# Kernel tuning notes

Hardware: AMD Instinct MI355X
Metric: run time of the kernel (lower is better)

## Reference

```python
import jax, jax.numpy as jnp
import numpy as np


def _conv(x, w, b=None, stride=1, pad=0):
    y = jax.lax.conv_general_dilated(x, w, (stride, stride), [(pad, pad), (pad, pad)],
                                     dimension_numbers=('NCHW', 'OIHW', 'NCHW'))
    if b is not None:
        y = y + b[None, :, None, None]
    return y


def _slice3d(grid, guide):
    # Trilinear grid_sample, align_corners=False, zero padding.
    # grid: (N, C=12, D=8, GH, GW); guide: (N,1,H,W) in [-1,1]
    N, C, D, GH, GW = grid.shape
    H, W = guide.shape[2], guide.shape[3]
    xs = 2.0 * jnp.arange(W, dtype=grid.dtype) / max(W - 1, 1) - 1.0
    ys = 2.0 * jnp.arange(H, dtype=grid.dtype) / max(H - 1, 1) - 1.0
    gx = ((xs + 1.0) * GW - 1.0) * 0.5               # (W,)
    gy = ((ys + 1.0) * GH - 1.0) * 0.5               # (H,)
    gz = ((guide[:, 0] + 1.0) * D - 1.0) * 0.5       # (N,H,W)
    x0f = jnp.floor(gx); y0f = jnp.floor(gy); z0f = jnp.floor(gz)
    fx = gx - x0f; fy = gy - y0f; fz = gz - z0f
    x0 = x0f.astype(jnp.int32); y0 = y0f.astype(jnp.int32); z0 = z0f.astype(jnp.int32)
    gf = grid.reshape(N, C, D * GH * GW)

    def corner(zi, yi, xi, wz, wy, wx):
        mask = ((zi >= 0) & (zi < D)) & ((yi >= 0) & (yi < GH))[None, :, None] & ((xi >= 0) & (xi < GW))[None, None, :]
        zc = jnp.clip(zi, 0, D - 1); yc = jnp.clip(yi, 0, GH - 1); xc = jnp.clip(xi, 0, GW - 1)
        flat = zc * (GH * GW) + yc[None, :, None] * GW + xc[None, None, :]   # (N,H,W)
        v = jnp.take_along_axis(gf, flat.reshape(N, 1, H * W), axis=2).reshape(N, C, H, W)
        w = (wz * wy[None, :, None] * wx[None, None, :]) * mask.astype(grid.dtype)  # (N,H,W)
        return v * w[:, None]

    out = jnp.zeros((N, C, H, W), grid.dtype)
    for dz in (0, 1):
        for dy in (0, 1):
            for dx in (0, 1):
                out = out + corner(z0 + dz, y0 + dy, x0 + dx,
                                   fz if dz else 1.0 - fz,
                                   fy if dy else 1.0 - fy,
                                   fx if dx else 1.0 - fx)
    return out


def setup_inputs() -> dict:
    key = jax.random.key(0)
    ks = jax.random.split(key, 40)
    def w(i, shape):
        return jax.random.normal(ks[i], shape, jnp.float32) * 0.05
    return {
        'low_res': jax.random.uniform(ks[0], (4, 3, 256, 256), jnp.float32),
        'full_res': jax.random.uniform(ks[1], (4, 1, 1024, 1024), jnp.float32),
        'w0': w(2, (8, 3, 3, 3)), 'b0': w(3, (8,)),
        'w1': w(4, (16, 8, 3, 3)), 'b1': w(5, (16,)),
        'w2': w(6, (32, 16, 3, 3)), 'b2': w(7, (32,)),
        'w3': w(8, (64, 32, 3, 3)), 'b3': w(9, (64,)),
        'wl0': w(10, (64, 64, 3, 3)), 'bl0': w(11, (64,)),
        'wl1': w(12, (64, 64, 3, 3)),
        'wg1': w(13, (128, 64, 3, 3)), 'bg1': w(14, (128,)),
        'wg2': w(15, (256, 128, 3, 3)), 'bg2': w(16, (256,)),
        'wf1': w(17, (256, 448, 1, 1)), 'bf1': w(18, (256,)),
        'wf2': w(19, (128, 256, 1, 1)), 'bf2': w(20, (128,)),
        'wf3': w(21, (64, 128, 1, 1)), 'bf3': w(22, (64,)),
        'wlin': w(23, (96, 64, 1, 1)), 'blin': w(24, (96,)),
        'wgd1': w(25, (16, 1, 3, 3)), 'bgd1': w(26, (16,)),
        'wgd2': w(27, (1, 16, 1, 1)), 'bgd2': w(28, (1,)),
        'wau1': w(29, (16, 1, 1, 1)), 'bau1': w(30, (16,)),
        'wau2': w(31, (1, 16, 1, 1)), 'bau2': w(32, (1,)),
        'wav1': w(33, (16, 1, 1, 1)), 'bav1': w(34, (16,)),
        'wav2': w(35, (1, 16, 1, 1)), 'bav2': w(36, (1,)),
    }


def reference(low_res, full_res, w0, b0, w1, b1, w2, b2, w3, b3, wl0, bl0, wl1,
              wg1, bg1, wg2, bg2, wf1, bf1, wf2, bf2, wf3, bf3, wlin, blin,
              wgd1, bgd1, wgd2, bgd2, wau1, bau1, wau2, bau2, wav1, bav1, wav2, bav2):
    relu = jax.nn.relu
    N = low_res.shape[0]
    H, W = full_res.shape[2], full_res.shape[3]
    fake = jax.image.resize(low_res, (N, 3, H, W), 'bilinear')
    # splat stack: 4 stride-2 convs
    x = relu(_conv(low_res, w0, b0, 2, 1))
    x = relu(_conv(x, w1, b1, 2, 1))
    x = relu(_conv(x, w2, b2, 2, 1))
    splat = relu(_conv(x, w3, b3, 2, 1))                 # (N,64,16,16)
    local = _conv(relu(_conv(splat, wl0, bl0, 1, 1)), wl1, None, 1, 1)
    # global branch
    a0 = splat.mean(axis=(2, 3), keepdims=True)
    x1 = relu(_conv(splat, wg1, bg1, 2, 1))
    a1 = x1.mean(axis=(2, 3), keepdims=True)
    x2 = relu(_conv(x1, wg2, bg2, 2, 1))
    a2 = x2.mean(axis=(2, 3), keepdims=True)
    a = jnp.concatenate([a0, a1, a2], axis=1)            # (N,448,1,1)
    a = relu(_conv(a, wf1, bf1))
    a = relu(_conv(a, wf2, bf2))
    glob = relu(_conv(a, wf3, bf3))                      # (N,64,1,1)
    fused = relu(glob + local)
    fused = _conv(fused, wlin, blin)                     # (N,96,16,16)
    grid = fused.reshape(N, 12, 8, fused.shape[2], fused.shape[3])
    guidemap = jnp.tanh(_conv(relu(_conv(full_res, wgd1, bgd1, 1, 1)), wgd2, bgd2))
    coeff = _slice3d(grid, guidemap)                     # (N,12,H,W)
    Y = full_res * coeff[:, 3:4] + coeff[:, 0:3].sum(axis=1, keepdims=True)
    U0 = full_res * coeff[:, 7:8] + coeff[:, 4:7].sum(axis=1, keepdims=True)
    V0 = full_res * coeff[:, 11:12] + coeff[:, 8:11].sum(axis=1, keepdims=True)
    U = jnp.tanh(_conv(relu(_conv(U0, wau1, bau1)), wau2, bau2)) + fake[:, 1:2]
    V = jnp.tanh(_conv(relu(_conv(V0, wav1, bav1)), wav2, bav2)) + fake[:, 2:3]
    return jnp.concatenate([Y, U, V], axis=1)
```

## Files before the change

### kernel.cpp

```cpp
#include <hip/hip_runtime.h>
#include <math.h>


__device__ __forceinline__ float tanh_fast(float x) {
    float e = __expf(2.0f * x);
    return 1.0f - 2.0f / (e + 1.0f);
}

template<int CIN, int COUT, int HIN, int WIN, int HOUT, int WOUT>
__global__ __launch_bounds__(256) void conv_s2_small(
    const float* __restrict__ in, const float* __restrict__ w,
    const float* __restrict__ b, float* __restrict__ out)
{
    int idx = blockIdx.x * 256 + threadIdx.x;
    int wo = idx % WOUT; int t = idx / WOUT;
    int ho = t % HOUT; t /= HOUT;
    int co = t % COUT; int n = t / COUT;
    float acc = b[co];
    int hi0 = ho * 2 - 1, wi0 = wo * 2 - 1;
    const float* wp = w + (size_t)co * CIN * 9;
    #pragma unroll
    for (int ci = 0; ci < CIN; ++ci) {
        const float* ip = in + ((size_t)(n * CIN + ci)) * HIN * WIN;
        const float* wc = wp + ci * 9;
        #pragma unroll
        for (int kh = 0; kh < 3; ++kh) {
            int hi = hi0 + kh;
            if ((unsigned)hi >= (unsigned)HIN) continue;
            const float* row = ip + hi * WIN;
            #pragma unroll
            for (int kw = 0; kw < 3; ++kw) {
                int wi = wi0 + kw;
                if ((unsigned)wi >= (unsigned)WIN) continue;
                acc = fmaf(wc[kh * 3 + kw], row[wi], acc);
            }
        }
    }
    out[idx] = fmaxf(acc, 0.0f);
}

template<int CIN, int PARTS, int STRIDE, bool RELU, bool HASB,
         int COUT, int HIN, int WIN, int HOUT, int WOUT>
__device__ __forceinline__ void conv_p_dev(
    const float* __restrict__ in, const float* __restrict__ w,
    const float* __restrict__ b, float* __restrict__ out,
    int tb, float* red)
{
    constexpr int CPT = CIN / PARTS;
    constexpr int OPB = 256 / PARTS;
    int part = threadIdx.x / OPB;
    int oidx = threadIdx.x % OPB;
    int o = tb * OPB + oidx;
    int wo = o % WOUT; int t = o / WOUT;
    int ho = t % HOUT; t /= HOUT;
    int co = t % COUT; int n = t / COUT;
    int hi0 = ho * STRIDE - 1, wi0 = wo * STRIDE - 1;
    const float* wp = w + ((size_t)co * CIN + part * CPT) * 9;
    const float* ip = in + ((size_t)n * CIN + part * CPT) * HIN * WIN;
    float acc = 0.0f;
    #pragma unroll
    for (int ci = 0; ci < CPT; ++ci) {
        const float* ic = ip + (size_t)ci * HIN * WIN;
        const float* wc = wp + ci * 9;
        #pragma unroll
        for (int kh = 0; kh < 3; ++kh) {
            int hi = hi0 + kh;
            if ((unsigned)hi >= (unsigned)HIN) continue;
            const float* row = ic + hi * WIN;
            #pragma unroll
            for (int kw = 0; kw < 3; ++kw) {
                int wi = wi0 + kw;
                if ((unsigned)wi >= (unsigned)WIN) continue;
                acc = fmaf(wc[kh * 3 + kw], row[wi], acc);
            }
        }
    }
    red[threadIdx.x] = acc;
    __syncthreads();
    if (part == 0) {
        float s = acc;
        #pragma unroll
        for (int p = 1; p < PARTS; ++p) s += red[p * OPB + oidx];
        if (HASB) s += b[co];
        if (RELU) s = fmaxf(s, 0.0f);
        out[o] = s;
    }
}

__global__ __launch_bounds__(256) void conv2_k(
    const float* __restrict__ in, const float* __restrict__ w,
    const float* __restrict__ b, float* __restrict__ out)
{
    __shared__ float red[256];
    conv_p_dev<16, 4, 2, true, true, 32, 64, 64, 32, 32>(in, w, b, out, blockIdx.x, red);
}

__global__ __launch_bounds__(256) void conv3_k(
    const float* __restrict__ in, const float* __restrict__ w,
    const float* __restrict__ b, float* __restrict__ out)
{
    __shared__ float red[256];
    conv_p_dev<32, 8, 2, true, true, 64, 32, 32, 16, 16>(in, w, b, out, blockIdx.x, red);
}

__global__ __launch_bounds__(256) void k5_l0_g1_means(
    const float* __restrict__ splat,
    const float* __restrict__ wl0, const float* __restrict__ bl0, float* __restrict__ l0o,
    const float* __restrict__ wg1, const float* __restrict__ bg1, float* __restrict__ x1,
    float* __restrict__ avec)
{
    __shared__ float red[256];
    int bid = blockIdx.x;
    if (bid < 4096) {
        conv_p_dev<64, 16, 1, true, true, 64, 16, 16, 16, 16>(splat, wl0, bl0, l0o, bid, red);
    } else if (bid < 6144) {
        conv_p_dev<64, 16, 2, true, true, 128, 16, 16, 8, 8>(splat, wg1, bg1, x1, bid - 4096, red);
    } else {
        int wid = (bid - 6144) * 4 + (threadIdx.x >> 6);
        int lane = threadIdx.x & 63;
        int n = wid >> 6, c = wid & 63;
        const float* p = splat + ((size_t)(n * 64 + c)) * 256;
        float s = p[lane] + p[lane + 64] + p[lane + 128] + p[lane + 192];
        #pragma unroll
        for (int off = 32; off; off >>= 1) s += __shfl_down(s, off, 64);
        if (lane == 0) avec[n * 448 + c] = s * (1.0f / 256.0f);
    }
}

__global__ __launch_bounds__(256) void k6_l1_g2_means(
    const float* __restrict__ l0o, const float* __restrict__ wl1, float* __restrict__ localb,
    const float* __restrict__ x1, const float* __restrict__ wg2,
    const float* __restrict__ bg2, float* __restrict__ x2,
    float* __restrict__ avec)
{
    __shared__ float red[256];
    int bid = blockIdx.x;
    if (bid < 4096) {
        conv_p_dev<64, 16, 1, false, false, 64, 16, 16, 16, 16>(l0o, wl1, nullptr, localb, bid, red);
    } else if (bid < 5120) {
        conv_p_dev<128, 16, 2, true, true, 256, 8, 8, 4, 4>(x1, wg2, bg2, x2, bid - 4096, red);
    } else {
        int wid = (bid - 5120) * 4 + (threadIdx.x >> 6);
        int lane = threadIdx.x & 63;
        int n = wid >> 7, c = wid & 127;
        const float* p = x1 + ((size_t)(n * 128 + c)) * 64;
        float s = p[lane];
        #pragma unroll
        for (int off = 32; off; off >>= 1) s += __shfl_down(s, off, 64);
        if (lane == 0) avec[n * 448 + 64 + c] = s * (1.0f / 64.0f);
    }
}

__global__ __launch_bounds__(256) void kfc_fuse(
    const float* __restrict__ avec, const float* __restrict__ x2,
    const float* __restrict__ wf1, const float* __restrict__ bf1,
    const float* __restrict__ wf2, const float* __restrict__ bf2,
    const float* __restrict__ wf3, const float* __restrict__ bf3,
    const float* __restrict__ local,
    const float* __restrict__ wlin, const float* __restrict__ blin,
    float* __restrict__ grid)
{
    __shared__ float a[448];
    __shared__ float h1[256];
    __shared__ float h2[128];
    __shared__ float gl[64];
    int n = blockIdx.x / 96; int k = blockIdx.x % 96; int t = threadIdx.x;
    if (t < 192) a[t] = avec[n * 448 + t];
    {
        const float* p = x2 + ((size_t)(n * 256 + t)) * 16;
        float s = 0.0f;
        #pragma unroll
        for (int i = 0; i < 16; ++i) s += p[i];
        a[192 + t] = s * (1.0f / 16.0f);
    }
    __syncthreads();
    {
        float a0 = 0, a1 = 0, a2 = 0, a3 = 0;
        const float* wp = wf1 + (size_t)t * 448;
        for (int i = 0; i < 448; i += 4) {
            a0 = fmaf(wp[i], a[i], a0); a1 = fmaf(wp[i + 1], a[i + 1], a1);
            a2 = fmaf(wp[i + 2], a[i + 2], a2); a3 = fmaf(wp[i + 3], a[i + 3], a3);
        }
        h1[t] = fmaxf(a0 + a1 + a2 + a3 + bf1[t], 0.0f);
    }
    __syncthreads();
    if (t < 128) {
        float a0 = 0, a1 = 0, a2 = 0, a3 = 0;
        const float* wp = wf2 + (size_t)t * 256;
        for (int i = 0; i < 256; i += 4) {
            a0 = fmaf(wp[i], h1[i], a0); a1 = fmaf(wp[i + 1], h1[i + 1], a1);
            a2 = fmaf(wp[i + 2], h1[i + 2], a2); a3 = fmaf(wp[i + 3], h1[i + 3], a3);
        }
        h2[t] = fmaxf(a0 + a1 + a2 + a3 + bf2[t], 0.0f);
    }
    __syncthreads();
    if (t < 64) {
        float a0 = 0, a1 = 0, a2 = 0, a3 = 0;
        const float* wp = wf3 + (size_t)t * 128;
        for (int i = 0; i < 128; i += 4) {
            a0 = fmaf(wp[i], h2[i], a0); a1 = fmaf(wp[i + 1], h2[i + 1], a1);
            a2 = fmaf(wp[i + 2], h2[i + 2], a2); a3 = fmaf(wp[i + 3], h2[i + 3], a3);
        }
        gl[t] = fmaxf(a0 + a1 + a2 + a3 + bf3[t], 0.0f);
    }
    __syncthreads();
    float acc = blin[k];
    const float* wp = wlin + k * 64;
    const float* lo = local + (size_t)n * 64 * 256 + t;
    #pragma unroll 8
    for (int c = 0; c < 64; ++c)
        acc = fmaf(wp[c], fmaxf(gl[c] + lo[c * 256], 0.0f), acc);
    int ch = k >> 3; int z = k & 7;
    grid[(size_t)n * 24576 + (size_t)t * 96 + z * 12 + ch] = acc;
}

__global__ __launch_bounds__(256) void hdr_out_v3(
    const float* __restrict__ full, const float* __restrict__ low,
    const float* __restrict__ grid,
    const float* __restrict__ wgd1, const float* __restrict__ bgd1,
    const float* __restrict__ wgd2, const float* __restrict__ bgd2,
    const float* __restrict__ wau1, const float* __restrict__ bau1,
    const float* __restrict__ wau2, const float* __restrict__ bau2,
    const float* __restrict__ wav1, const float* __restrict__ bav1,
    const float* __restrict__ wav2, const float* __restrict__ bav2,
    float* __restrict__ out)
{
    int tid = blockIdx.x * 256 + threadIdx.x;
    int x = tid & 1023;
    int y = (tid >> 10) & 1023;
    int n = tid >> 20;
    const float* fp = full + ((size_t)n << 20);

    float v[3][3];
    #pragma unroll
    for (int r = 0; r < 3; ++r) {
        int yy = y + r - 1;
        bool okr = (unsigned)yy < 1024u;
        const float* row = fp + (size_t)yy * 1024;
        v[r][0] = (okr && x > 0)    ? row[x - 1] : 0.0f;
        v[r][1] = okr               ? row[x]     : 0.0f;
        v[r][2] = (okr && x < 1023) ? row[x + 1] : 0.0f;
    }

    float gacc = bgd2[0];
    #pragma unroll
    for (int k = 0; k < 16; ++k) {
        const float* wk = wgd1 + k * 9;
        float h = bgd1[k];
        h = fmaf(wk[0], v[0][0], h); h = fmaf(wk[1], v[0][1], h); h = fmaf(wk[2], v[0][2], h);
        h = fmaf(wk[3], v[1][0], h); h = fmaf(wk[4], v[1][1], h); h = fmaf(wk[5], v[1][2], h);
        h = fmaf(wk[6], v[2][0], h); h = fmaf(wk[7], v[2][1], h); h = fmaf(wk[8], v[2][2], h);
        gacc = fmaf(wgd2[k], fmaxf(h, 0.0f), gacc);
    }
    float g = tanh_fast(gacc);

    float gxc = (x * (32.0f / 1023.0f) - 1.0f) * 0.5f;
    float gyc = (y * (32.0f / 1023.0f) - 1.0f) * 0.5f;
    float gzc = 4.0f * g + 3.5f;
    float x0f = floorf(gxc), y0f = floorf(gyc), z0f = floorf(gzc);
    float fx = gxc - x0f, fy = gyc - y0f, fz = gzc - z0f;
    int ix = (int)x0f, iy = (int)y0f, iz = (int)z0f;

    float wx0 = (ix >= 0 && ix < 16) ? (1.0f - fx) : 0.0f;
    float wx1 = (ix + 1 < 16) ? fx : 0.0f;
    float wy0 = (iy >= 0 && iy < 16) ? (1.0f - fy) : 0.0f;
    float wy1 = (iy + 1 < 16) ? fy : 0.0f;
    float wz0 = (iz >= 0 && iz < 8) ? (1.0f - fz) : 0.0f;
    float wz1 = (iz + 1 >= 0 && iz + 1 < 8) ? fz : 0.0f;
    int xi0 = min(max(ix, 0), 15), xi1 = min(ix + 1, 15);
    int yi0 = min(max(iy, 0), 15), yi1 = min(iy + 1, 15);
    int zi0 = min(max(iz, 0), 7),  zi1 = min(max(iz + 1, 0), 7);

    float w00 = wy0 * wx0, w01 = wy0 * wx1, w10 = wy1 * wx0, w11 = wy1 * wx1;

    const float* gb = grid + (size_t)n * 24576;
    const float* c00 = gb + (yi0 * 16 + xi0) * 96;
    const float* c01 = gb + (yi0 * 16 + xi1) * 96;
    const float* c10 = gb + (yi1 * 16 + xi0) * 96;
    const float* c11 = gb + (yi1 * 16 + xi1) * 96;
    int zo0 = zi0 * 12;
    int zo1 = zi1 * 12;

    float acc[12];
    #pragma unroll
    for (int i = 0; i < 12; ++i) acc[i] = 0.0f;

    #define CORNER(PTR, WK) { \
        const float4* q = (const float4*)(PTR); \
        float wk_ = (WK); \
        float4 A = q[0], B = q[1], C = q[2]; \
        acc[0] = fmaf(wk_, A.x, acc[0]); acc[1] = fmaf(wk_, A.y, acc[1]); \
        acc[2] = fmaf(wk_, A.z, acc[2]); acc[3] = fmaf(wk_, A.w, acc[3]); \
        acc[4] = fmaf(wk_, B.x, acc[4]); acc[5] = fmaf(wk_, B.y, acc[5]); \
        acc[6] = fmaf(wk_, B.z, acc[6]); acc[7] = fmaf(wk_, B.w, acc[7]); \
        acc[8] = fmaf(wk_, C.x, acc[8]); acc[9] = fmaf(wk_, C.y, acc[9]); \
        acc[10] = fmaf(wk_, C.z, acc[10]); acc[11] = fmaf(wk_, C.w, acc[11]); }

    CORNER(c00 + zo0, wz0 * w00)
    CORNER(c01 + zo0, wz0 * w01)
    CORNER(c10 + zo0, wz0 * w10)
    CORNER(c11 + zo0, wz0 * w11)
    CORNER(c00 + zo1, wz1 * w00)
    CORNER(c01 + zo1, wz1 * w01)
    CORNER(c10 + zo1, wz1 * w10)
    CORNER(c11 + zo1, wz1 * w11)
    #undef CORNER

    float p = v[1][1];
    float Yv = fmaf(p, acc[3],  acc[0] + acc[1] + acc[2]);
    float U0 = fmaf(p, acc[7],  acc[4] + acc[5] + acc[6]);
    float V0 = fmaf(p, acc[11], acc[8] + acc[9] + acc[10]);

    float uacc = bau2[0];
    #pragma unroll
    for (int k = 0; k < 16; ++k)
        uacc = fmaf(wau2[k], fmaxf(fmaf(wau1[k], U0, bau1[k]), 0.0f), uacc);
    float vacc = bav2[0];
    #pragma unroll
    for (int k = 0; k < 16; ++k)
        vacc = fmaf(wav2[k], fmaxf(fmaf(wav1[k], V0, bav1[k]), 0.0f), vacc);

    float sx = (x + 0.5f) * 0.25f - 0.5f;
    float sy = (y + 0.5f) * 0.25f - 0.5f;
    float sxf = floorf(sx), syf = floorf(sy);
    float fxl = sx - sxf, fyl = sy - syf;
    int jx0 = max((int)sxf, 0), jx1 = min((int)sxf + 1, 255);
    int jy0 = max((int)syf, 0), jy1 = min((int)syf + 1, 255);
    const float* lr1 = low + ((size_t)(n * 3 + 1)) * 65536;
    const float* lr2 = low + ((size_t)(n * 3 + 2)) * 65536;
    float f1 = (1.0f - fyl) * ((1.0f - fxl) * lr1[jy0 * 256 + jx0] + fxl * lr1[jy0 * 256 + jx1])
             + fyl * ((1.0f - fxl) * lr1[jy1 * 256 + jx0] + fxl * lr1[jy1 * 256 + jx1]);
    float f2 = (1.0f - fyl) * ((1.0f - fxl) * lr2[jy0 * 256 + jx0] + fxl * lr2[jy0 * 256 + jx1])
             + fyl * ((1.0f - fxl) * lr2[jy1 * 256 + jx0] + fxl * lr2[jy1 * 256 + jx1]);

    float Uv = tanh_fast(uacc) + f1;
    float Vv = tanh_fast(vacc) + f2;

    size_t base = ((size_t)n * 3) * 1048576 + (size_t)y * 1024 + x;
    out[base]            = Yv;
    out[base + 1048576]  = Uv;
    out[base + 2097152]  = Vv;
}

extern "C" void kernel_launch(void* const* d_in, const int* in_sizes, int n_in,
                              void* d_out, int out_size, void* d_ws, size_t ws_size,
                              hipStream_t stream)
{
    const float* low  = (const float*)d_in[0];
    const float* full = (const float*)d_in[1];
    const float* w0 = (const float*)d_in[2];  const float* b0 = (const float*)d_in[3];
    const float* w1 = (const float*)d_in[4];  const float* b1 = (const float*)d_in[5];
    const float* w2 = (const float*)d_in[6];  const float* b2 = (const float*)d_in[7];
    const float* w3 = (const float*)d_in[8];  const float* b3 = (const float*)d_in[9];
    const float* wl0 = (const float*)d_in[10]; const float* bl0 = (const float*)d_in[11];
    const float* wl1 = (const float*)d_in[12];
    const float* wg1 = (const float*)d_in[13]; const float* bg1 = (const float*)d_in[14];
    const float* wg2 = (const float*)d_in[15]; const float* bg2 = (const float*)d_in[16];
    const float* wf1 = (const float*)d_in[17]; const float* bf1 = (const float*)d_in[18];
    const float* wf2 = (const float*)d_in[19]; const float* bf2 = (const float*)d_in[20];
    const float* wf3 = (const float*)d_in[21]; const float* bf3 = (const float*)d_in[22];
    const float* wlin = (const float*)d_in[23]; const float* blin = (const float*)d_in[24];
    const float* wgd1 = (const float*)d_in[25]; const float* bgd1 = (const float*)d_in[26];
    const float* wgd2 = (const float*)d_in[27]; const float* bgd2 = (const float*)d_in[28];
    const float* wau1 = (const float*)d_in[29]; const float* bau1 = (const float*)d_in[30];
    const float* wau2 = (const float*)d_in[31]; const float* bau2 = (const float*)d_in[32];
    const float* wav1 = (const float*)d_in[33]; const float* bav1 = (const float*)d_in[34];
    const float* wav2 = (const float*)d_in[35]; const float* bav2 = (const float*)d_in[36];
    float* out = (float*)d_out;

    float* ws = (float*)d_ws;
    float* t0b    = ws;
    float* t1b    = t0b + 524288;
    float* t2b    = t1b + 262144;
    float* splat  = t2b + 131072;
    float* l0o    = splat + 65536;
    float* localb = l0o + 65536;
    float* x1b    = localb + 65536;
    float* x2b    = x1b + 32768;
    float* avec   = x2b + 16384;
    float* gridb  = avec + 1792;

    conv_s2_small<3, 8, 256, 256, 128, 128><<<2048, 256, 0, stream>>>(low, w0, b0, t0b);
    conv_s2_small<8, 16, 128, 128, 64, 64><<<1024, 256, 0, stream>>>(t0b, w1, b1, t1b);
    conv2_k<<<2048, 256, 0, stream>>>(t1b, w2, b2, t2b);
    conv3_k<<<2048, 256, 0, stream>>>(t2b, w3, b3, splat);
    k5_l0_g1_means<<<6208, 256, 0, stream>>>(splat, wl0, bl0, l0o, wg1, bg1, x1b, avec);
    k6_l1_g2_means<<<5248, 256, 0, stream>>>(l0o, wl1, localb, x1b, wg2, bg2, x2b, avec);
    kfc_fuse<<<384, 256, 0, stream>>>(avec, x2b, wf1, bf1, wf2, bf2, wf3, bf3,
                                      localb, wlin, blin, gridb);
    hdr_out_v3<<<16384, 256, 0, stream>>>(full, low, gridb,
        wgd1, bgd1, wgd2, bgd2, wau1, bau1, wau2, bau2, wav1, bav1, wav2, bav2, out);
}
```

Before: 352.2 us.

## Fuse low-res pipeline stages into one persistent cooperative kernel with grid syncs

```diff
diff --git a/kernel.cpp b/kernel.cpp
--- a/kernel.cpp
+++ b/kernel.cpp
@@ -1,5 +1,8 @@
 #include <hip/hip_runtime.h>
+#include <hip/hip_cooperative_groups.h>
 #include <math.h>
+
+namespace cg = cooperative_groups;
 
 
 __device__ __forceinline__ float tanh_fast(float x) {
@@ -8,11 +11,11 @@
 }
 
 template<int CIN, int COUT, int HIN, int WIN, int HOUT, int WOUT>
-__global__ __launch_bounds__(256) void conv_s2_small(
+__device__ __forceinline__ void conv_s2_dev(
     const float* __restrict__ in, const float* __restrict__ w,
-    const float* __restrict__ b, float* __restrict__ out)
-{
-    int idx = blockIdx.x * 256 + threadIdx.x;
+    const float* __restrict__ b, float* __restrict__ out, int wb)
+{
+    int idx = wb * 256 + (int)threadIdx.x;
     int wo = idx % WOUT; int t = idx / WOUT;
     int ho = t % HOUT; t /= HOUT;
     int co = t % COUT; int n = t / COUT;
@@ -87,36 +90,20 @@
     }
 }
 
-__global__ __launch_bounds__(256) void conv2_k(
-    const float* __restrict__ in, const float* __restrict__ w,
-    const float* __restrict__ b, float* __restrict__ out)
-{
-    __shared__ float red[256];
-    conv_p_dev<16, 4, 2, true, true, 32, 64, 64, 32, 32>(in, w, b, out, blockIdx.x, red);
-}
-
-__global__ __launch_bounds__(256) void conv3_k(
-    const float* __restrict__ in, const float* __restrict__ w,
-    const float* __restrict__ b, float* __restrict__ out)
-{
-    __shared__ float red[256];
-    conv_p_dev<32, 8, 2, true, true, 64, 32, 32, 16, 16>(in, w, b, out, blockIdx.x, red);
-}
-
-__global__ __launch_bounds__(256) void k5_l0_g1_means(
+__device__ __forceinline__ void k5_dev(
     const float* __restrict__ splat,
     const float* __restrict__ wl0, const float* __restrict__ bl0, float* __restrict__ l0o,
     const float* __restrict__ wg1, const float* __restrict__ bg1, float* __restrict__ x1,
-    float* __restrict__ avec)
-{
-    __shared__ float red[256];
-    int bid = blockIdx.x;
+    float* __restrict__ avec, float* red, int bid)
+{
     if (bid < 4096) {
         conv_p_dev<64, 16, 1, true, true, 64, 16, 16, 16, 16>(splat, wl0, bl0, l0o, bid, red);
+        __syncthreads();
     } else if (bid < 6144) {
         conv_p_dev<64, 16, 2, true, true, 128, 16, 16, 8, 8>(splat, wg1, bg1, x1, bid - 4096, red);
+        __syncthreads();
     } else {
-        int wid = (bid - 6144) * 4 + (threadIdx.x >> 6);
+        int wid = (bid - 6144) * 4 + ((int)threadIdx.x >> 6);
         int lane = threadIdx.x & 63;
         int n = wid >> 6, c = wid & 63;
         const float* p = splat + ((size_t)(n * 64 + c)) * 256;
@@ -127,20 +114,20 @@
     }
 }
 
-__global__ __launch_bounds__(256) void k6_l1_g2_means(
+__device__ __forceinline__ void k6_dev(
     const float* __restrict__ l0o, const float* __restrict__ wl1, float* __restrict__ localb,
     const float* __restrict__ x1, const float* __restrict__ wg2,
     const float* __restrict__ bg2, float* __restrict__ x2,
-    float* __restrict__ avec)
-{
-    __shared__ float red[256];
-    int bid = blockIdx.x;
+    float* __restrict__ avec, float* red, int bid)
+{
     if (bid < 4096) {
         conv_p_dev<64, 16, 1, false, false, 64, 16, 16, 16, 16>(l0o, wl1, nullptr, localb, bid, red);
+        __syncthreads();
     } else if (bid < 5120) {
         conv_p_dev<128, 16, 2, true, true, 256, 8, 8, 4, 4>(x1, wg2, bg2, x2, bid - 4096, red);
+        __syncthreads();
     } else {
-        int wid = (bid - 5120) * 4 + (threadIdx.x >> 6);
+        int wid = (bid - 5120) * 4 + ((int)threadIdx.x >> 6);
         int lane = threadIdx.x & 63;
         int n = wid >> 7, c = wid & 127;
         const float* p = x1 + ((size_t)(n * 128 + c)) * 64;
@@ -151,7 +138,168 @@
     }
 }
 
-__global__ __launch_bounds__(256) void kfc_fuse(
+__device__ __forceinline__ void kfc_dev(
+    const float* __restrict__ avec, const float* __restrict__ x2,
+    const float* __restrict__ wf1, const float* __restrict__ bf1,
+    const float* __restrict__ wf2, const float* __restrict__ bf2,
+    const float* __restrict__ wf3, const float* __restrict__ bf3,
+    const float* __restrict__ local,
+    const float* __restrict__ wlin, const float* __restrict__ blin,
+    float* __restrict__ grid, int wk)
+{
+    __shared__ float a[448];
+    __shared__ float h1[256];
+    __shared__ float h2[128];
+    __shared__ float gl[64];
+    int n = wk / 96; int k = wk % 96; int t = threadIdx.x;
+    if (t < 192) a[t] = avec[n * 448 + t];
+    {
+        const float* p = x2 + ((size_t)(n * 256 + t)) * 16;
+        float s = 0.0f;
+        #pragma unroll
+        for (int i = 0; i < 16; ++i) s += p[i];
+        a[192 + t] = s * (1.0f / 16.0f);
+    }
+    __syncthreads();
+    {
+        float a0 = 0, a1 = 0, a2 = 0, a3 = 0;
+        const float* wp = wf1 + (size_t)t * 448;
+        for (int i = 0; i < 448; i += 4) {
+            a0 = fmaf(wp[i], a[i], a0); a1 = fmaf(wp[i + 1], a[i + 1], a1);
+            a2 = fmaf(wp[i + 2], a[i + 2], a2); a3 = fmaf(wp[i + 3], a[i + 3], a3);
+        }
+        h1[t] = fmaxf(a0 + a1 + a2 + a3 + bf1[t], 0.0f);
+    }
+    __syncthreads();
+    if (t < 128) {
+        float a0 = 0, a1 = 0, a2 = 0, a3 = 0;
+        const float* wp = wf2 + (size_t)t * 256;
+        for (int i = 0; i < 256; i += 4) {
+            a0 = fmaf(wp[i], h1[i], a0); a1 = fmaf(wp[i + 1], h1[i + 1], a1);
+            a2 = fmaf(wp[i + 2], h1[i + 2], a2); a3 = fmaf(wp[i + 3], h1[i + 3], a3);
+        }
+        h2[t] = fmaxf(a0 + a1 + a2 + a3 + bf2[t], 0.0f);
+    }
+    __syncthreads();
+    if (t < 64) {
+        float a0 = 0, a1 = 0, a2 = 0, a3 = 0;
+        const float* wp = wf3 + (size_t)t * 128;
+        for (int i = 0; i < 128; i += 4) {
+            a0 = fmaf(wp[i], h2[i], a0); a1 = fmaf(wp[i + 1], h2[i + 1], a1);
+            a2 = fmaf(wp[i + 2], h2[i + 2], a2); a3 = fmaf(wp[i + 3], h2[i + 3], a3);
+        }
+        gl[t] = fmaxf(a0 + a1 + a2 + a3 + bf3[t], 0.0f);
+    }
+    __syncthreads();
+    float acc = blin[k];
+    const float* wp = wlin + k * 64;
+    const float* lo = local + (size_t)n * 64 * 256 + t;
+    #pragma unroll 8
+    for (int c = 0; c < 64; ++c)
+        acc = fmaf(wp[c], fmaxf(gl[c] + lo[c * 256], 0.0f), acc);
+    grid[(size_t)n * 24576 + (size_t)t * 96 + (k & 7) * 12 + (k >> 3)] = acc;
+    __syncthreads();
+}
+
+__global__ __launch_bounds__(256) void lowres_pipe(
+    const float* __restrict__ low,
+    const float* __restrict__ w0, const float* __restrict__ b0,
+    const float* __restrict__ w1, const float* __restrict__ b1,
+    const float* __restrict__ w2, const float* __restrict__ b2,
+    const float* __restrict__ w3, const float* __restrict__ b3,
+    const float* __restrict__ wl0, const float* __restrict__ bl0,
+    const float* __restrict__ wl1,
+    const float* __restrict__ wg1, const float* __restrict__ bg1,
+    const float* __restrict__ wg2, const float* __restrict__ bg2,
+    const float* __restrict__ wf1, const float* __restrict__ bf1,
+    const float* __restrict__ wf2, const float* __restrict__ bf2,
+    const float* __restrict__ wf3, const float* __restrict__ bf3,
+    const float* __restrict__ wlin, const float* __restrict__ blin,
+    float* __restrict__ ws)
+{
+    cg::grid_group gg = cg::this_grid();
+    __shared__ float red[256];
+    float* t0b    = ws;
+    float* t1b    = t0b + 524288;
+    float* t2b    = t1b + 262144;
+    float* splat  = t2b + 131072;
+    float* l0o    = splat + 65536;
+    float* localb = l0o + 65536;
+    float* x1b    = localb + 65536;
+    float* x2b    = x1b + 32768;
+    float* avec   = x2b + 16384;
+    float* gridb  = avec + 1792;
+    const int G = gridDim.x;
+
+    for (int wb = blockIdx.x; wb < 2048; wb += G)
+        conv_s2_dev<3, 8, 256, 256, 128, 128>(low, w0, b0, t0b, wb);
+    gg.sync();
+    for (int wb = blockIdx.x; wb < 1024; wb += G)
+        conv_s2_dev<8, 16, 128, 128, 64, 64>(t0b, w1, b1, t1b, wb);
+    gg.sync();
+    for (int wb = blockIdx.x; wb < 2048; wb += G) {
+        conv_p_dev<16, 4, 2, true, true, 32, 64, 64, 32, 32>(t1b, w2, b2, t2b, wb, red);
+        __syncthreads();
+    }
+    gg.sync();
+    for (int wb = blockIdx.x; wb < 2048; wb += G) {
+        conv_p_dev<32, 8, 2, true, true, 64, 32, 32, 16, 16>(t2b, w3, b3, splat, wb, red);
+        __syncthreads();
+    }
+    gg.sync();
+    for (int wb = blockIdx.x; wb < 6208; wb += G)
+        k5_dev(splat, wl0, bl0, l0o, wg1, bg1, x1b, avec, red, wb);
+    gg.sync();
+    for (int wb = blockIdx.x; wb < 5248; wb += G)
+        k6_dev(l0o, wl1, localb, x1b, wg2, bg2, x2b, avec, red, wb);
+    gg.sync();
+    for (int wb = blockIdx.x; wb < 384; wb += G)
+        kfc_dev(avec, x2b, wf1, bf1, wf2, bf2, wf3, bf3, localb, wlin, blin, gridb, wb);
+}
+
+template<int CIN, int COUT, int HIN, int WIN, int HOUT, int WOUT>
+__global__ __launch_bounds__(256) void conv_s2_g(
+    const float* __restrict__ in, const float* __restrict__ w,
+    const float* __restrict__ b, float* __restrict__ out)
+{ conv_s2_dev<CIN, COUT, HIN, WIN, HOUT, WOUT>(in, w, b, out, blockIdx.x); }
+
+__global__ __launch_bounds__(256) void conv2_g(
+    const float* __restrict__ in, const float* __restrict__ w,
+    const float* __restrict__ b, float* __restrict__ out)
+{
+    __shared__ float red[256];
+    conv_p_dev<16, 4, 2, true, true, 32, 64, 64, 32, 32>(in, w, b, out, blockIdx.x, red);
+}
+
+__global__ __launch_bounds__(256) void conv3_g(
+    const float* __restrict__ in, const float* __restrict__ w,
+    const float* __restrict__ b, float* __restrict__ out)
+{
+    __shared__ float red[256];
+    conv_p_dev<32, 8, 2, true, true, 64, 32, 32, 16, 16>(in, w, b, out, blockIdx.x, red);
+}
+
+__global__ __launch_bounds__(256) void k5_g(
+    const float* __restrict__ splat,
+    const float* __restrict__ wl0, const float* __restrict__ bl0, float* __restrict__ l0o,
+    const float* __restrict__ wg1, const float* __restrict__ bg1, float* __restrict__ x1,
+    float* __restrict__ avec)
+{
+    __shared__ float red[256];
+    k5_dev(splat, wl0, bl0, l0o, wg1, bg1, x1, avec, red, blockIdx.x);
+}
+
+__global__ __launch_bounds__(256) void k6_g(
+    const float* __restrict__ l0o, const float* __restrict__ wl1, float* __restrict__ localb,
+    const float* __restrict__ x1, const float* __restrict__ wg2,
+    const float* __restrict__ bg2, float* __restrict__ x2,
+    float* __restrict__ avec)
+{
+    __shared__ float red[256];
+    k6_dev(l0o, wl1, localb, x1, wg2, bg2, x2, avec, red, blockIdx.x);
+}
+
+__global__ __launch_bounds__(256) void kfc_g(
     const float* __restrict__ avec, const float* __restrict__ x2,
     const float* __restrict__ wf1, const float* __restrict__ bf1,
     const float* __restrict__ wf2, const float* __restrict__ bf2,
@@ -160,58 +308,7 @@
     const float* __restrict__ wlin, const float* __restrict__ blin,
     float* __restrict__ grid)
 {
-    __shared__ float a[448];
-    __shared__ float h1[256];
-    __shared__ float h2[128];
-    __shared__ float gl[64];
-    int n = blockIdx.x / 96; int k = blockIdx.x % 96; int t = threadIdx.x;
-    if (t < 192) a[t] = avec[n * 448 + t];
-    {
-        const float* p = x2 + ((size_t)(n * 256 + t)) * 16;
-        float s = 0.0f;
-        #pragma unroll
-        for (int i = 0; i < 16; ++i) s += p[i];
-        a[192 + t] = s * (1.0f / 16.0f);
-    }
-    __syncthreads();
-    {
-        float a0 = 0, a1 = 0, a2 = 0, a3 = 0;
-        const float* wp = wf1 + (size_t)t * 448;
-        for (int i = 0; i < 448; i += 4) {
-            a0 = fmaf(wp[i], a[i], a0); a1 = fmaf(wp[i + 1], a[i + 1], a1);
-            a2 = fmaf(wp[i + 2], a[i + 2], a2); a3 = fmaf(wp[i + 3], a[i + 3], a3);
-        }
-        h1[t] = fmaxf(a0 + a1 + a2 + a3 + bf1[t], 0.0f);
-    }
-    __syncthreads();
-    if (t < 128) {
-        float a0 = 0, a1 = 0, a2 = 0, a3 = 0;
-        const float* wp = wf2 + (size_t)t * 256;
-        for (int i = 0; i < 256; i += 4) {
-            a0 = fmaf(wp[i], h1[i], a0); a1 = fmaf(wp[i + 1], h1[i + 1], a1);
-            a2 = fmaf(wp[i + 2], h1[i + 2], a2); a3 = fmaf(wp[i + 3], h1[i + 3], a3);
-        }
-        h2[t] = fmaxf(a0 + a1 + a2 + a3 + bf2[t], 0.0f);
-    }
-    __syncthreads();
-    if (t < 64) {
-        float a0 = 0, a1 = 0, a2 = 0, a3 = 0;
-        const float* wp = wf3 + (size_t)t * 128;
-        for (int i = 0; i < 128; i += 4) {
-            a0 = fmaf(wp[i], h2[i], a0); a1 = fmaf(wp[i + 1], h2[i + 1], a1);
-            a2 = fmaf(wp[i + 2], h2[i + 2], a2); a3 = fmaf(wp[i + 3], h2[i + 3], a3);
-        }
-        gl[t] = fmaxf(a0 + a1 + a2 + a3 + bf3[t], 0.0f);
-    }
-    __syncthreads();
-    float acc = blin[k];
-    const float* wp = wlin + k * 64;
-    const float* lo = local + (size_t)n * 64 * 256 + t;
-    #pragma unroll 8
-    for (int c = 0; c < 64; ++c)
-        acc = fmaf(wp[c], fmaxf(gl[c] + lo[c * 256], 0.0f), acc);
-    int ch = k >> 3; int z = k & 7;
-    grid[(size_t)n * 24576 + (size_t)t * 96 + z * 12 + ch] = acc;
+    kfc_dev(avec, x2, wf1, bf1, wf2, bf2, wf3, bf3, local, wlin, blin, grid, blockIdx.x);
 }
 
 __global__ __launch_bounds__(256) void hdr_out_v3(
@@ -380,14 +477,52 @@
     float* avec   = x2b + 16384;
     float* gridb  = avec + 1792;
 
-    conv_s2_small<3, 8, 256, 256, 128, 128><<<2048, 256, 0, stream>>>(low, w0, b0, t0b);
-    conv_s2_small<8, 16, 128, 128, 64, 64><<<1024, 256, 0, stream>>>(t0b, w1, b1, t1b);
-    conv2_k<<<2048, 256, 0, stream>>>(t1b, w2, b2, t2b);
-    conv3_k<<<2048, 256, 0, stream>>>(t2b, w3, b3, splat);
-    k5_l0_g1_means<<<6208, 256, 0, stream>>>(splat, wl0, bl0, l0o, wg1, bg1, x1b, avec);
-    k6_l1_g2_means<<<5248, 256, 0, stream>>>(l0o, wl1, localb, x1b, wg2, bg2, x2b, avec);
-    kfc_fuse<<<384, 256, 0, stream>>>(avec, x2b, wf1, bf1, wf2, bf2, wf3, bf3,
-                                      localb, wlin, blin, gridb);
+    static int coopG = -1;
+    if (coopG == -1) {
+        int nb = 0;
+        if (hipOccupancyMaxActiveBlocksPerMultiprocessor(&nb, lowres_pipe, 256, 0) == hipSuccess
+            && nb > 0) {
+            int g = nb * 256;
+            if (g > 1024) g = 1024;
+            coopG = g;
+        } else {
+            coopG = 0;
+        }
+    }
+
+    bool fused = false;
+    if (coopG > 0) {
+        void* args[] = {
+            (void*)&low,
+            (void*)&w0, (void*)&b0, (void*)&w1, (void*)&b1,
+            (void*)&w2, (void*)&b2, (void*)&w3, (void*)&b3,
+            (void*)&wl0, (void*)&bl0, (void*)&wl1,
+            (void*)&wg1, (void*)&bg1, (void*)&wg2, (void*)&bg2,
+            (void*)&wf1, (void*)&bf1, (void*)&wf2, (void*)&bf2,
+            (void*)&wf3, (void*)&bf3, (void*)&wlin, (void*)&blin,
+            (void*)&ws
+        };
+        hipError_t err = hipLaunchCooperativeKernel(lowres_pipe, dim3(coopG), dim3(256),
+                                                    args, 0, stream);
+        if (err == hipSuccess) {
+            fused = true;
+        } else {
+            (void)hipGetLastError();
+            coopG = 0;
+        }
+    }
+
+    if (!fused) {
+        conv_s2_g<3, 8, 256, 256, 128, 128><<<2048, 256, 0, stream>>>(low, w0, b0, t0b);
+        conv_s2_g<8, 16, 128, 128, 64, 64><<<1024, 256, 0, stream>>>(t0b, w1, b1, t1b);
+        conv2_g<<<2048, 256, 0, stream>>>(t1b, w2, b2, t2b);
+        conv3_g<<<2048, 256, 0, stream>>>(t2b, w3, b3, splat);
+        k5_g<<<6208, 256, 0, stream>>>(splat, wl0, bl0, l0o, wg1, bg1, x1b, avec);
+        k6_g<<<5248, 256, 0, stream>>>(l0o, wl1, localb, x1b, wg2, bg2, x2b, avec);
+        kfc_g<<<384, 256, 0, stream>>>(avec, x2b, wf1, bf1, wf2, bf2, wf3, bf3,
+                                       localb, wlin, blin, gridb);
+    }
+
     hdr_out_v3<<<16384, 256, 0, stream>>>(full, low, gridb,
         wgd1, bgd1, wgd2, bgd2, wau1, bau1, wau2, bau2, wav1, bav1, wav2, bav2, out);
 }
```

Result: slower. 801.5 us (+127.6%).

## Fuse low-res pipeline into one persistent kernel with grid-wide barriers

Applied to the files above, without the earlier changes.

```diff
diff --git a/kernel.cpp b/kernel.cpp
--- a/kernel.cpp
+++ b/kernel.cpp
@@ -8,11 +8,11 @@
 }
 
 template<int CIN, int COUT, int HIN, int WIN, int HOUT, int WOUT>
-__global__ __launch_bounds__(256) void conv_s2_small(
+__device__ __forceinline__ void conv_s2_dev(
     const float* __restrict__ in, const float* __restrict__ w,
-    const float* __restrict__ b, float* __restrict__ out)
-{
-    int idx = blockIdx.x * 256 + threadIdx.x;
+    const float* __restrict__ b, float* __restrict__ out, int wb)
+{
+    int idx = wb * 256 + (int)threadIdx.x;
     int wo = idx % WOUT; int t = idx / WOUT;
     int ho = t % HOUT; t /= HOUT;
     int co = t % COUT; int n = t / COUT;
@@ -87,36 +87,20 @@
     }
 }
 
-__global__ __launch_bounds__(256) void conv2_k(
-    const float* __restrict__ in, const float* __restrict__ w,
-    const float* __restrict__ b, float* __restrict__ out)
-{
-    __shared__ float red[256];
-    conv_p_dev<16, 4, 2, true, true, 32, 64, 64, 32, 32>(in, w, b, out, blockIdx.x, red);
-}
-
-__global__ __launch_bounds__(256) void conv3_k(
-    const float* __restrict__ in, const float* __restrict__ w,
-    const float* __restrict__ b, float* __restrict__ out)
-{
-    __shared__ float red[256];
-    conv_p_dev<32, 8, 2, true, true, 64, 32, 32, 16, 16>(in, w, b, out, blockIdx.x, red);
-}
-
-__global__ __launch_bounds__(256) void k5_l0_g1_means(
+__device__ __forceinline__ void k5_dev(
     const float* __restrict__ splat,
     const float* __restrict__ wl0, const float* __restrict__ bl0, float* __restrict__ l0o,
     const float* __restrict__ wg1, const float* __restrict__ bg1, float* __restrict__ x1,
-    float* __restrict__ avec)
-{
-    __shared__ float red[256];
-    int bid = blockIdx.x;
+    float* __restrict__ avec, float* red, int bid)
+{
     if (bid < 4096) {
         conv_p_dev<64, 16, 1, true, true, 64, 16, 16, 16, 16>(splat, wl0, bl0, l0o, bid, red);
+        __syncthreads();
     } else if (bid < 6144) {
         conv_p_dev<64, 16, 2, true, true, 128, 16, 16, 8, 8>(splat, wg1, bg1, x1, bid - 4096, red);
+        __syncthreads();
     } else {
-        int wid = (bid - 6144) * 4 + (threadIdx.x >> 6);
+        int wid = (bid - 6144) * 4 + ((int)threadIdx.x >> 6);
         int lane = threadIdx.x & 63;
         int n = wid >> 6, c = wid & 63;
         const float* p = splat + ((size_t)(n * 64 + c)) * 256;
@@ -127,20 +111,20 @@
     }
 }
 
-__global__ __launch_bounds__(256) void k6_l1_g2_means(
+__device__ __forceinline__ void k6_dev(
     const float* __restrict__ l0o, const float* __restrict__ wl1, float* __restrict__ localb,
     const float* __restrict__ x1, const float* __restrict__ wg2,
     const float* __restrict__ bg2, float* __restrict__ x2,
-    float* __restrict__ avec)
-{
-    __shared__ float red[256];
-    int bid = blockIdx.x;
+    float* __restrict__ avec, float* red, int bid)
+{
     if (bid < 4096) {
         conv_p_dev<64, 16, 1, false, false, 64, 16, 16, 16, 16>(l0o, wl1, nullptr, localb, bid, red);
+        __syncthreads();
     } else if (bid < 5120) {
         conv_p_dev<128, 16, 2, true, true, 256, 8, 8, 4, 4>(x1, wg2, bg2, x2, bid - 4096, red);
+        __syncthreads();
     } else {
-        int wid = (bid - 5120) * 4 + (threadIdx.x >> 6);
+        int wid = (bid - 5120) * 4 + ((int)threadIdx.x >> 6);
         int lane = threadIdx.x & 63;
         int n = wid >> 7, c = wid & 127;
         const float* p = x1 + ((size_t)(n * 128 + c)) * 64;
@@ -151,20 +135,20 @@
     }
 }
 
-__global__ __launch_bounds__(256) void kfc_fuse(
+__device__ __forceinline__ void kfc_dev(
     const float* __restrict__ avec, const float* __restrict__ x2,
     const float* __restrict__ wf1, const float* __restrict__ bf1,
     const float* __restrict__ wf2, const float* __restrict__ bf2,
     const float* __restrict__ wf3, const float* __restrict__ bf3,
     const float* __restrict__ local,
     const float* __restrict__ wlin, const float* __restrict__ blin,
-    float* __restrict__ grid)
+    float* __restrict__ grid, int wk)
 {
     __shared__ float a[448];
     __shared__ float h1[256];
     __shared__ float h2[128];
     __shared__ float gl[64];
-    int n = blockIdx.x / 96; int k = blockIdx.x % 96; int t = threadIdx.x;
+    int n = wk / 96; int k = wk % 96; int t = threadIdx.x;
     if (t < 192) a[t] = avec[n * 448 + t];
     {
         const float* p = x2 + ((size_t)(n * 256 + t)) * 16;
@@ -210,8 +194,78 @@
     #pragma unroll 8
     for (int c = 0; c < 64; ++c)
         acc = fmaf(wp[c], fmaxf(gl[c] + lo[c * 256], 0.0f), acc);
-    int ch = k >> 3; int z = k & 7;
-    grid[(size_t)n * 24576 + (size_t)t * 96 + z * 12 + ch] = acc;
+    grid[(size_t)n * 24576 + (size_t)t * 96 + (k & 7) * 12 + (k >> 3)] = acc;
+    __syncthreads();
+}
+
+__device__ __forceinline__ void gbar(unsigned* cnt, unsigned target)
+{
+    __syncthreads();
+    if (threadIdx.x == 0) {
+        __threadfence();
+        __hip_atomic_fetch_add(cnt, 1u, __ATOMIC_RELEASE, __HIP_MEMORY_SCOPE_AGENT);
+        while (__hip_atomic_load(cnt, __ATOMIC_ACQUIRE, __HIP_MEMORY_SCOPE_AGENT) < target)
+            __builtin_amdgcn_s_sleep(4);
+        __threadfence();
+    }
+    __syncthreads();
+}
+
+__global__ __launch_bounds__(256) void lowres_fused(
+    const float* __restrict__ low,
+    const float* __restrict__ w0, const float* __restrict__ b0,
+    const float* __restrict__ w1, const float* __restrict__ b1,
+    const float* __restrict__ w2, const float* __restrict__ b2,
+    const float* __restrict__ w3, const float* __restrict__ b3,
+    const float* __restrict__ wl0, const float* __restrict__ bl0,
+    const float* __restrict__ wl1,
+    const float* __restrict__ wg1, const float* __restrict__ bg1,
+    const float* __restrict__ wg2, const float* __restrict__ bg2,
+    const float* __restrict__ wf1, const float* __restrict__ bf1,
+    const float* __restrict__ wf2, const float* __restrict__ bf2,
+    const float* __restrict__ wf3, const float* __restrict__ bf3,
+    const float* __restrict__ wlin, const float* __restrict__ blin,
+    float* __restrict__ ws)
+{
+    __shared__ float red[256];
+    float* t0b    = ws;
+    float* t1b    = t0b + 524288;
+    float* t2b    = t1b + 262144;
+    float* splat  = t2b + 131072;
+    float* l0o    = splat + 65536;
+    float* localb = l0o + 65536;
+    float* x1b    = localb + 65536;
+    float* x2b    = x1b + 32768;
+    float* avec   = x2b + 16384;
+    float* gridb  = avec + 1792;
+    unsigned* cnt = (unsigned*)(gridb + 98304);
+    const int G = gridDim.x;
+    const unsigned uG = (unsigned)G;
+
+    for (int wb = blockIdx.x; wb < 2048; wb += G)
+        conv_s2_dev<3, 8, 256, 256, 128, 128>(low, w0, b0, t0b, wb);
+    gbar(cnt, uG * 1u);
+    for (int wb = blockIdx.x; wb < 1024; wb += G)
+        conv_s2_dev<8, 16, 128, 128, 64, 64>(t0b, w1, b1, t1b, wb);
+    gbar(cnt, uG * 2u);
+    for (int wb = blockIdx.x; wb < 2048; wb += G) {
+        conv_p_dev<16, 4, 2, true, true, 32, 64, 64, 32, 32>(t1b, w2, b2, t2b, wb, red);
+        __syncthreads();
+    }
+    gbar(cnt, uG * 3u);
+    for (int wb = blockIdx.x; wb < 2048; wb += G) {
+        conv_p_dev<32, 8, 2, true, true, 64, 32, 32, 16, 16>(t2b, w3, b3, splat, wb, red);
+        __syncthreads();
+    }
+    gbar(cnt, uG * 4u);
+    for (int wb = blockIdx.x; wb < 6208; wb += G)
+        k5_dev(splat, wl0, bl0, l0o, wg1, bg1, x1b, avec, red, wb);
+    gbar(cnt, uG * 5u);
+    for (int wb = blockIdx.x; wb < 5248; wb += G)
+        k6_dev(l0o, wl1, localb, x1b, wg2, bg2, x2b, avec, red, wb);
+    gbar(cnt, uG * 6u);
+    for (int wb = blockIdx.x; wb < 384; wb += G)
+        kfc_dev(avec, x2b, wf1, bf1, wf2, bf2, wf3, bf3, localb, wlin, blin, gridb, wb);
 }
 
 __global__ __launch_bounds__(256) void hdr_out_v3(
@@ -369,25 +423,17 @@
     float* out = (float*)d_out;
 
     float* ws = (float*)d_ws;
-    float* t0b    = ws;
-    float* t1b    = t0b + 524288;
-    float* t2b    = t1b + 262144;
-    float* splat  = t2b + 131072;
-    float* l0o    = splat + 65536;
-    float* localb = l0o + 65536;
-    float* x1b    = localb + 65536;
-    float* x2b    = x1b + 32768;
-    float* avec   = x2b + 16384;
-    float* gridb  = avec + 1792;
-
-    conv_s2_small<3, 8, 256, 256, 128, 128><<<2048, 256, 0, stream>>>(low, w0, b0, t0b);
-    conv_s2_small<8, 16, 128, 128, 64, 64><<<1024, 256, 0, stream>>>(t0b, w1, b1, t1b);
-    conv2_k<<<2048, 256, 0, stream>>>(t1b, w2, b2, t2b);
-    conv3_k<<<2048, 256, 0, stream>>>(t2b, w3, b3, splat);
-    k5_l0_g1_means<<<6208, 256, 0, stream>>>(splat, wl0, bl0, l0o, wg1, bg1, x1b, avec);
-    k6_l1_g2_means<<<5248, 256, 0, stream>>>(l0o, wl1, localb, x1b, wg2, bg2, x2b, avec);
-    kfc_fuse<<<384, 256, 0, stream>>>(avec, x2b, wf1, bf1, wf2, bf2, wf3, bf3,
-                                      localb, wlin, blin, gridb);
+    float* gridb = ws + 524288 + 262144 + 131072 + 65536 + 65536 + 65536
+                      + 32768 + 16384 + 1792;
+    void* cntb = (void*)(gridb + 98304);
+
+    hipMemsetAsync(cntb, 0, 256, stream);
+
+    lowres_fused<<<256, 256, 0, stream>>>(
+        low, w0, b0, w1, b1, w2, b2, w3, b3,
+        wl0, bl0, wl1, wg1, bg1, wg2, bg2,
+        wf1, bf1, wf2, bf2, wf3, bf3, wlin, blin, ws);
+
     hdr_out_v3<<<16384, 256, 0, stream>>>(full, low, gridb,
         wgd1, bgd1, wgd2, bgd2, wau1, bau1, wau2, bau2, wav1, bav1, wav2, bav2, out);
 }
```

After: 678.3 us. +92.6%, slower.

## Fuse four strided low-res convolutions into one tiled kernel with LDS halos

Applied to the files above, without the earlier changes.

```diff
diff --git a/kernel.cpp b/kernel.cpp
--- a/kernel.cpp
+++ b/kernel.cpp
@@ -7,36 +7,148 @@
     return 1.0f - 2.0f / (e + 1.0f);
 }
 
-template<int CIN, int COUT, int HIN, int WIN, int HOUT, int WOUT>
-__global__ __launch_bounds__(256) void conv_s2_small(
-    const float* __restrict__ in, const float* __restrict__ w,
-    const float* __restrict__ b, float* __restrict__ out)
-{
-    int idx = blockIdx.x * 256 + threadIdx.x;
-    int wo = idx % WOUT; int t = idx / WOUT;
-    int ho = t % HOUT; t /= HOUT;
-    int co = t % COUT; int n = t / COUT;
-    float acc = b[co];
-    int hi0 = ho * 2 - 1, wi0 = wo * 2 - 1;
-    const float* wp = w + (size_t)co * CIN * 9;
-    #pragma unroll
-    for (int ci = 0; ci < CIN; ++ci) {
-        const float* ip = in + ((size_t)(n * CIN + ci)) * HIN * WIN;
-        const float* wc = wp + ci * 9;
-        #pragma unroll
-        for (int kh = 0; kh < 3; ++kh) {
-            int hi = hi0 + kh;
-            if ((unsigned)hi >= (unsigned)HIN) continue;
-            const float* row = ip + hi * WIN;
+__global__ __launch_bounds__(256) void conv0123_fused(
+    const float* __restrict__ low,
+    const float* __restrict__ w0, const float* __restrict__ b0,
+    const float* __restrict__ w1, const float* __restrict__ b1,
+    const float* __restrict__ w2, const float* __restrict__ b2,
+    const float* __restrict__ w3, const float* __restrict__ b3,
+    float* __restrict__ splat)
+{
+    __shared__ float t0s[8 * 529];
+    __shared__ float t1s[16 * 121];
+    __shared__ float t2s[32 * 25];
+    const int tid = (int)threadIdx.x;
+    const int n  = blockIdx.x >> 6;
+    const int ty = (blockIdx.x >> 3) & 7;
+    const int tx = blockIdx.x & 7;
+    const int o0h = 16 * ty - 7, o0w = 16 * tx - 7;
+    const int o1h = 8 * ty - 3,  o1w = 8 * tx - 3;
+    const int o2h = 4 * ty - 1,  o2w = 4 * tx - 1;
+
+    const float* lown = low + (size_t)n * 3 * 65536;
+    for (int idx = tid; idx < 8 * 529; idx += 256) {
+        int c = idx / 529, p = idx - c * 529;
+        int r = p / 23, q = p - r * 23;
+        int h0 = o0h + r, w0g = o0w + q;
+        float v = 0.0f;
+        if ((unsigned)h0 < 128u && (unsigned)w0g < 128u) {
+            float acc = b0[c];
+            const float* wp = w0 + c * 27;
+            int hi0 = h0 * 2 - 1, wi0 = w0g * 2 - 1;
             #pragma unroll
-            for (int kw = 0; kw < 3; ++kw) {
-                int wi = wi0 + kw;
-                if ((unsigned)wi >= (unsigned)WIN) continue;
-                acc = fmaf(wc[kh * 3 + kw], row[wi], acc);
+            for (int ci = 0; ci < 3; ++ci) {
+                const float* ip = lown + ci * 65536;
+                const float* wc = wp + ci * 9;
+                #pragma unroll
+                for (int kh = 0; kh < 3; ++kh) {
+                    int hi = hi0 + kh;
+                    if ((unsigned)hi >= 256u) continue;
+                    const float* row = ip + hi * 256;
+                    #pragma unroll
+                    for (int kw = 0; kw < 3; ++kw) {
+                        int wi = wi0 + kw;
+                        if ((unsigned)wi >= 256u) continue;
+                        acc = fmaf(wc[kh * 3 + kw], row[wi], acc);
+                    }
+                }
             }
-        }
-    }
-    out[idx] = fmaxf(acc, 0.0f);
+            v = fmaxf(acc, 0.0f);
+        }
+        t0s[idx] = v;
+    }
+    __syncthreads();
+
+    for (int idx = tid; idx < 16 * 121; idx += 256) {
+        int c = idx / 121, p = idx - c * 121;
+        int r = p / 11, q = p - r * 11;
+        int h1 = o1h + r, w1g = o1w + q;
+        float v = 0.0f;
+        if ((unsigned)h1 < 64u && (unsigned)w1g < 64u) {
+            float acc = b1[c];
+            const float* wp = w1 + c * 72;
+            #pragma unroll
+            for (int ci = 0; ci < 8; ++ci) {
+                const float* tc = t0s + ci * 529;
+                const float* wc = wp + ci * 9;
+                #pragma unroll
+                for (int kh = 0; kh < 3; ++kh) {
+                    const float* rw = tc + (2 * r + kh) * 23 + 2 * q;
+                    acc = fmaf(wc[kh * 3 + 0], rw[0], acc);
+                    acc = fmaf(wc[kh * 3 + 1], rw[1], acc);
+                    acc = fmaf(wc[kh * 3 + 2], rw[2], acc);
+                }
+            }
+            v = fmaxf(acc, 0.0f);
+        }
+        t1s[idx] = v;
+    }
+    __syncthreads();
+
+    for (int idx = tid; idx < 32 * 25; idx += 256) {
+        int c = idx / 25, p = idx - c * 25;
+        int r = p / 5, q = p - r * 5;
+        int h2 = o2h + r, w2g = o2w + q;
+        float v = 0.0f;
+        if ((unsigned)h2 < 32u && (unsigned)w2g < 32u) {
+            const float* wp = w2 + c * 144;
+            float ps0 = 0, ps1 = 0, ps2 = 0, ps3 = 0;
+            #pragma unroll
+            for (int part = 0; part < 4; ++part) {
+                float a = 0.0f;
+                #pragma unroll
+                for (int cc = 0; cc < 4; ++cc) {
+                    int ci = part * 4 + cc;
+                    const float* tc = t1s + ci * 121;
+                    const float* wc = wp + ci * 9;
+                    #pragma unroll
+                    for (int kh = 0; kh < 3; ++kh) {
+                        const float* rw = tc + (2 * r + kh) * 11 + 2 * q;
+                        a = fmaf(wc[kh * 3 + 0], rw[0], a);
+                        a = fmaf(wc[kh * 3 + 1], rw[1], a);
+                        a = fmaf(wc[kh * 3 + 2], rw[2], a);
+                    }
+                }
+                if (part == 0) ps0 = a; else if (part == 1) ps1 = a;
+                else if (part == 2) ps2 = a; else ps3 = a;
+            }
+            float s = ps0; s += ps1; s += ps2; s += ps3;
+            s += b2[c];
+            v = fmaxf(s, 0.0f);
+        }
+        t2s[idx] = v;
+    }
+    __syncthreads();
+
+    {
+        int c = tid >> 2, sh = (tid >> 1) & 1, sw = tid & 1;
+        int ho = 2 * ty + sh, wo = 2 * tx + sw;
+        const float* wp = w3 + c * 288;
+        float parts[8];
+        #pragma unroll
+        for (int part = 0; part < 8; ++part) {
+            float a = 0.0f;
+            #pragma unroll
+            for (int cc = 0; cc < 4; ++cc) {
+                int ci = part * 4 + cc;
+                const float* tc = t2s + ci * 25;
+                const float* wc = wp + ci * 9;
+                #pragma unroll
+                for (int kh = 0; kh < 3; ++kh) {
+                    const float* rw = tc + (2 * sh + kh) * 5 + 2 * sw;
+                    a = fmaf(wc[kh * 3 + 0], rw[0], a);
+                    a = fmaf(wc[kh * 3 + 1], rw[1], a);
+                    a = fmaf(wc[kh * 3 + 2], rw[2], a);
+                }
+            }
+            parts[part] = a;
+        }
+        float s = parts[0];
+        #pragma unroll
+        for (int p = 1; p < 8; ++p) s += parts[p];
+        s += b3[c];
+        splat[(((size_t)(n * 64 + c)) * 16 + ho) * 16 + wo] = fmaxf(s, 0.0f);
+    }
 }
 
 template<int CIN, int PARTS, int STRIDE, bool RELU, bool HASB,
@@ -87,22 +199,6 @@
     }
 }
 
-__global__ __launch_bounds__(256) void conv2_k(
-    const float* __restrict__ in, const float* __restrict__ w,
-    const float* __restrict__ b, float* __restrict__ out)
-{
-    __shared__ float red[256];
-    conv_p_dev<16, 4, 2, true, true, 32, 64, 64, 32, 32>(in, w, b, out, blockIdx.x, red);
-}
-
-__global__ __launch_bounds__(256) void conv3_k(
-    const float* __restrict__ in, const float* __restrict__ w,
-    const float* __restrict__ b, float* __restrict__ out)
-{
-    __shared__ float red[256];
-    conv_p_dev<32, 8, 2, true, true, 64, 32, 32, 16, 16>(in, w, b, out, blockIdx.x, red);
-}
-
 __global__ __launch_bounds__(256) void k5_l0_g1_means(
     const float* __restrict__ splat,
     const float* __restrict__ wl0, const float* __restrict__ bl0, float* __restrict__ l0o,
@@ -116,7 +212,7 @@
     } else if (bid < 6144) {
         conv_p_dev<64, 16, 2, true, true, 128, 16, 16, 8, 8>(splat, wg1, bg1, x1, bid - 4096, red);
     } else {
-        int wid = (bid - 6144) * 4 + (threadIdx.x >> 6);
+        int wid = (bid - 6144) * 4 + ((int)threadIdx.x >> 6);
         int lane = threadIdx.x & 63;
         int n = wid >> 6, c = wid & 63;
         const float* p = splat + ((size_t)(n * 64 + c)) * 256;
@@ -140,7 +236,7 @@
     } else if (bid < 5120) {
         conv_p_dev<128, 16, 2, true, true, 256, 8, 8, 4, 4>(x1, wg2, bg2, x2, bid - 4096, red);
     } else {
-        int wid = (bid - 5120) * 4 + (threadIdx.x >> 6);
+        int wid = (bid - 5120) * 4 + ((int)threadIdx.x >> 6);
         int lane = threadIdx.x & 63;
         int n = wid >> 7, c = wid & 127;
         const float* p = x1 + ((size_t)(n * 128 + c)) * 64;
@@ -210,8 +306,7 @@
     #pragma unroll 8
     for (int c = 0; c < 64; ++c)
         acc = fmaf(wp[c], fmaxf(gl[c] + lo[c * 256], 0.0f), acc);
-    int ch = k >> 3; int z = k & 7;
-    grid[(size_t)n * 24576 + (size_t)t * 96 + z * 12 + ch] = acc;
+    grid[(size_t)n * 24576 + (size_t)t * 96 + (k & 7) * 12 + (k >> 3)] = acc;
 }
 
 __global__ __launch_bounds__(256) void hdr_out_v3(
@@ -379,11 +474,9 @@
     float* x2b    = x1b + 32768;
     float* avec   = x2b + 16384;
     float* gridb  = avec + 1792;
-
-    conv_s2_small<3, 8, 256, 256, 128, 128><<<2048, 256, 0, stream>>>(low, w0, b0, t0b);
-    conv_s2_small<8, 16, 128, 128, 64, 64><<<1024, 256, 0, stream>>>(t0b, w1, b1, t1b);
-    conv2_k<<<2048, 256, 0, stream>>>(t1b, w2, b2, t2b);
-    conv3_k<<<2048, 256, 0, stream>>>(t2b, w3, b3, splat);
+    (void)t0b; (void)t1b;
+
+    conv0123_fused<<<256, 256, 0, stream>>>(low, w0, b0, w1, b1, w2, b2, w3, b3, splat);
     k5_l0_g1_means<<<6208, 256, 0, stream>>>(splat, wl0, bl0, l0o, wg1, bg1, x1b, avec);
     k6_l1_g2_means<<<5248, 256, 0, stream>>>(l0o, wl1, localb, x1b, wg2, bg2, x2b, avec);
     kfc_fuse<<<384, 256, 0, stream>>>(avec, x2b, wf1, bf1, wf2, bf2, wf3, bf3,
```

Result: no change. 357.3 us (+1.5%).
